# Kernel optimization log

Hardware: AMD Instinct MI355X
Metric: run time of the kernel (lower is better)

The kernel has to match this reference:

```python
import jax, jax.numpy as jnp
import numpy as np

B, C, F, T = 4, 64, 256, 256
CH = C // 2  # self.n_ch inside the module
EPS = 1e-5


def _cbp(x, W, b, g, be, m, v, a):
    # 1x1 conv == channel matmul, then BatchNorm (inference stats) + PReLU (scalar slope)
    y = jnp.einsum('oi,bift->boft', W, x) + b[None, :, None, None]
    y = (y - m[None, :, None, None]) * jax.lax.rsqrt(v[None, :, None, None] + EPS)
    y = y * g[None, :, None, None] + be[None, :, None, None]
    return jnp.where(y > 0, y, a * y)


def setup_inputs() -> dict:
    key = jax.random.key(0)
    ks = jax.random.split(key, 16)

    def conv_params(i, cin, cout, pre):
        W = jax.random.normal(ks[i], (cout, cin), dtype=jnp.float32) * 0.05
        return {
            pre + '_W': W,
            pre + '_b': jnp.zeros((cout,), jnp.float32),
            pre + '_g': jnp.ones((cout,), jnp.float32),
            pre + '_be': jnp.zeros((cout,), jnp.float32),
            pre + '_m': jax.random.normal(ks[i + 1], (cout,), dtype=jnp.float32) * 0.1,
            pre + '_v': jax.random.uniform(ks[i + 2], (cout,), dtype=jnp.float32) + 0.5,
            pre + '_a': jnp.float32(0.25),
        }

    d = {
        'inp': jax.random.normal(ks[12], (B, C, F, T), dtype=jnp.float32),
        'x': jax.random.normal(ks[13], (B, C, F, T), dtype=jnp.float32),
    }
    d.update(conv_params(0, C, 2 * CH, 'fqk'))
    d.update(conv_params(3, C, CH, 'fv'))
    d.update(conv_params(6, C, 2 * CH, 'tqk'))
    d.update(conv_params(9, CH, C, 'proj'))
    return d


def reference(inp, x,
              fqk_W, fqk_b, fqk_g, fqk_be, fqk_m, fqk_v, fqk_a,
              fv_W, fv_b, fv_g, fv_be, fv_m, fv_v, fv_a,
              tqk_W, tqk_b, tqk_g, tqk_be, tqk_m, tqk_v, tqk_a,
              proj_W, proj_b, proj_g, proj_be, proj_m, proj_v, proj_a):
    scale = 1.0 / jnp.sqrt(jnp.float32(CH))

    # frequency attention
    f_qk = _cbp(inp, fqk_W, fqk_b, fqk_g, fqk_be, fqk_m, fqk_v, fqk_a)  # B,2CH,F,T
    vf = _cbp(x, fv_W, fv_b, fv_g, fv_be, fv_m, fv_v, fv_a)             # B,CH,F,T
    r = f_qk.reshape(f_qk.shape[0], CH, 2, F, T)  # 'b (c k) f t -> b c k f t'
    qf, kf = r[:, :, 0], r[:, :, 1]
    f_score = jnp.einsum('bcft,bcyt->btfy', qf, kf) * scale
    f_score = jax.nn.softmax(f_score, axis=-1)
    fout = jnp.einsum('btfy,bcyt->bcft', f_score, vf)

    # time attention (causal mask)
    t_qk = _cbp(inp, tqk_W, tqk_b, tqk_g, tqk_be, tqk_m, tqk_v, tqk_a)
    r = t_qk.reshape(t_qk.shape[0], CH, 2, F, T)
    qt, kt = r[:, :, 0], r[:, :, 1]
    t_score = jnp.einsum('bcft,bcfy->bfty', qt, kt) * scale
    mask = jnp.triu(jnp.ones((T, T), dtype=bool), k=1)  # j - i + 1 with i == j
    neg = -jnp.finfo(t_score.dtype).max
    t_score = jnp.where(mask, neg, t_score)
    t_score = jax.nn.softmax(t_score, axis=-1)
    tout = jnp.einsum('bfty,bcfy->bcft', t_score, fout)

    out = _cbp(tout, proj_W, proj_b, proj_g, proj_be, proj_m, proj_v, proj_a)
    return out + x
```

## Files before the change

kernel.cpp:

```cpp
#include <hip/hip_runtime.h>
#include <hip/hip_bf16.h>

typedef __hip_bfloat16 bf16;
typedef __attribute__((ext_vector_type(8))) short bf16x8;
typedef __attribute__((ext_vector_type(4))) float f32x4;
typedef __attribute__((ext_vector_type(16))) float f32x16;
typedef __attribute__((ext_vector_type(8))) unsigned short u16x8;
typedef __attribute__((ext_vector_type(4))) unsigned int u32x4;
typedef __attribute__((ext_vector_type(2))) unsigned int u32x2;

struct ConvP {
  const float* W; const float* bi; const float* g; const float* be;
  const float* m; const float* v; const float* a;
};

#define QS (0.17677669529663687f * 1.4426950408889634f)

__device__ __forceinline__ unsigned short f2bf(float f) {
  __hip_bfloat16 h = __float2bfloat16(f);
  return __builtin_bit_cast(unsigned short, h);
}
__device__ __forceinline__ float bf2f(unsigned short u) {
  return __uint_as_float(((unsigned)u) << 16);
}
__device__ __forceinline__ float fast_exp2(float x) {
#if __has_builtin(__builtin_amdgcn_exp2f)
  return __builtin_amdgcn_exp2f(x);
#else
  return exp2f(x);
#endif
}

__global__ __launch_bounds__(256, 2) void conv_qkv(
    const float* __restrict__ inp, const float* __restrict__ x,
    ConvP fqk, ConvP fv, ConvP tqk,
    bf16* __restrict__ Qf, bf16* __restrict__ Kf, bf16* __restrict__ Vf,
    bf16* __restrict__ Qt, bf16* __restrict__ Kt)
{
  __shared__ __attribute__((aligned(16))) unsigned short Xb[64 * 260];
  __shared__ __attribute__((aligned(16))) unsigned short S0[256 * 40];
  __shared__ __attribute__((aligned(16))) unsigned short S1[256 * 40];
  __shared__ __attribute__((aligned(8)))  float2 Pc[160];

  const int tid = threadIdx.x;
  const int b = blockIdx.x >> 8;
  const int f = blockIdx.x & 255;
  const size_t gbase = (size_t)b * 64 * 65536 + f * 256;
  const size_t tbase = (size_t)(b * 256 + f) * 8192;

  const int lane = tid & 63;
  const int wid = tid >> 6;
  const int m16 = lane & 15;
  const int quad = lane >> 4;

  if (tid < 160) {
    const ConvP& P = (tid < 64) ? fqk : (tid < 128) ? tqk : fv;
    const int o = (tid < 64) ? tid : (tid < 128) ? tid - 64 : tid - 128;
    float A = P.g[o] * rsqrtf(P.v[o] + 1e-5f);
    float B2 = (P.bi[o] - P.m[o]) * A + P.be[o];
    if (tid < 128 && ((o & 1) == 0)) { A *= QS; B2 *= QS; }
    Pc[tid] = make_float2(A, B2);
  }

  auto load_X = [&](const float* __restrict__ src) {
    #pragma unroll
    for (int r = 0; r < 16; ++r) {
      const int idx = r * 256 + tid;
      const int c = idx >> 6;
      const int t0 = (idx & 63) * 4;
      const float4 v = *(const float4*)(src + gbase + (size_t)c * 65536 + t0);
      unsigned lo = (unsigned)f2bf(v.x) | (((unsigned)f2bf(v.y)) << 16);
      unsigned hi = (unsigned)f2bf(v.z) | (((unsigned)f2bf(v.w)) << 16);
      u32x2 pk = {lo, hi};
      *(u32x2*)&Xb[c * 260 + t0] = pk;
    }
  };

  auto load_A = [&](const float* __restrict__ W, int rowbase, int ks) {
    const float* p = W + (rowbase + m16) * 64 + ks * 32 + quad * 8;
    const float4 lo = *(const float4*)p;
    const float4 hi = *(const float4*)(p + 4);
    bf16x8 r;
    r[0] = (short)f2bf(lo.x); r[1] = (short)f2bf(lo.y);
    r[2] = (short)f2bf(lo.z); r[3] = (short)f2bf(lo.w);
    r[4] = (short)f2bf(hi.x); r[5] = (short)f2bf(hi.y);
    r[6] = (short)f2bf(hi.z); r[7] = (short)f2bf(hi.w);
    return r;
  };

  auto load_B = [&](int tt, int ks) {
    const int t = tt * 16 + m16;
    const int i0 = ks * 32 + quad * 8;
    bf16x8 r;
    #pragma unroll
    for (int j = 0; j < 8; ++j) r[j] = (short)Xb[(i0 + j) * 260 + t];
    return r;
  };

  auto emit = [&](const unsigned short* S, bf16* __restrict__ dst) {
    #pragma unroll
    for (int r = 0; r < 4; ++r) {
      const int chunk = r * 256 + tid;
      const int t = chunk >> 2, part = chunk & 3;
      u32x4 v = *(const u32x4*)&S[t * 40 + part * 8];
      *(u32x4*)(dst + tbase + (size_t)chunk * 8) = v;
    }
  };

  auto leaky = [](float y, float alpha) { return y > 0.f ? y : alpha * y; };

  auto qk_pass = [&](const ConvP& P, int pcb, const bf16x8 (&Bf)[4][2]) {
    bf16x8 A[4][2];
    #pragma unroll
    for (int ot = 0; ot < 4; ++ot)
      #pragma unroll
      for (int ks = 0; ks < 2; ++ks) A[ot][ks] = load_A(P.W, ot * 16, ks);
    float pA[4][4], pB[4][4];
    #pragma unroll
    for (int ot = 0; ot < 4; ++ot)
      #pragma unroll
      for (int r = 0; r < 4; ++r) {
        const float2 pp = Pc[pcb + ot * 16 + quad * 4 + r];
        pA[ot][r] = pp.x; pB[ot][r] = pp.y;
      }
    const float alpha = P.a[0];
    #pragma unroll
    for (int i = 0; i < 4; ++i) {
      const int t = (wid * 4 + i) * 16 + m16;
      #pragma unroll
      for (int ot = 0; ot < 4; ++ot) {
        f32x4 acc = {0.f, 0.f, 0.f, 0.f};
        acc = __builtin_amdgcn_mfma_f32_16x16x32_bf16(A[ot][0], Bf[i][0], acc, 0, 0, 0);
        acc = __builtin_amdgcn_mfma_f32_16x16x32_bf16(A[ot][1], Bf[i][1], acc, 0, 0, 0);
        float y[4];
        #pragma unroll
        for (int r = 0; r < 4; ++r)
          y[r] = leaky(acc[r] * pA[ot][r] + pB[ot][r], alpha);
        const int ch0 = ot * 8 + quad * 2;
        *(unsigned*)&S0[t * 40 + ch0] = (unsigned)f2bf(y[0]) | (((unsigned)f2bf(y[2])) << 16);
        *(unsigned*)&S1[t * 40 + ch0] = (unsigned)f2bf(y[1]) | (((unsigned)f2bf(y[3])) << 16);
      }
    }
  };

  load_X(inp);
  __syncthreads();

  bf16x8 Bf[4][2];
  #pragma unroll
  for (int i = 0; i < 4; ++i)
    #pragma unroll
    for (int ks = 0; ks < 2; ++ks) Bf[i][ks] = load_B(wid * 4 + i, ks);

  qk_pass(fqk, 0, Bf);
  __syncthreads();
  emit(S0, Qf); emit(S1, Kf);
  __syncthreads();
  qk_pass(tqk, 64, Bf);
  __syncthreads();
  emit(S0, Qt); emit(S1, Kt);
  __syncthreads();
  load_X(x);
  __syncthreads();

  {
    bf16x8 A[2][2], Bv[4][2];
    #pragma unroll
    for (int i = 0; i < 4; ++i)
      #pragma unroll
      for (int ks = 0; ks < 2; ++ks) Bv[i][ks] = load_B(wid * 4 + i, ks);
    #pragma unroll
    for (int ot = 0; ot < 2; ++ot)
      #pragma unroll
      for (int ks = 0; ks < 2; ++ks) A[ot][ks] = load_A(fv.W, ot * 16, ks);
    float pA[2][4], pB[2][4];
    #pragma unroll
    for (int ot = 0; ot < 2; ++ot)
      #pragma unroll
      for (int r = 0; r < 4; ++r) {
        const float2 pp = Pc[128 + ot * 16 + quad * 4 + r];
        pA[ot][r] = pp.x; pB[ot][r] = pp.y;
      }
    const float alpha = fv.a[0];
    #pragma unroll
    for (int i = 0; i < 4; ++i) {
      const int t = (wid * 4 + i) * 16 + m16;
      #pragma unroll
      for (int ot = 0; ot < 2; ++ot) {
        f32x4 acc = {0.f, 0.f, 0.f, 0.f};
        acc = __builtin_amdgcn_mfma_f32_16x16x32_bf16(A[ot][0], Bv[i][0], acc, 0, 0, 0);
        acc = __builtin_amdgcn_mfma_f32_16x16x32_bf16(A[ot][1], Bv[i][1], acc, 0, 0, 0);
        float y[4];
        #pragma unroll
        for (int r = 0; r < 4; ++r)
          y[r] = leaky(acc[r] * pA[ot][r] + pB[ot][r], alpha);
        const int ch = ot * 16 + quad * 4;
        *(unsigned*)&S0[t * 40 + ch]     = (unsigned)f2bf(y[0]) | (((unsigned)f2bf(y[1])) << 16);
        *(unsigned*)&S0[t * 40 + ch + 2] = (unsigned)f2bf(y[2]) | (((unsigned)f2bf(y[3])) << 16);
      }
    }
  }
  __syncthreads();
  emit(S0, Vf);
}

template<bool CAUSAL>
__global__ __launch_bounds__(256, 2) void attn_k(
    const bf16* __restrict__ Qg, const bf16* __restrict__ Kg,
    const bf16* __restrict__ Vg, bf16* __restrict__ Og)
{
  __shared__ __attribute__((aligned(16))) unsigned short Kl[256 * 40];
  __shared__ __attribute__((aligned(16))) unsigned short Vt[32 * 264];
  __shared__ __attribute__((aligned(16))) unsigned short Plds[4][16 * 264];
  __shared__ __attribute__((aligned(16))) unsigned short Wsc[4][16 * 40];

  const int inst = blockIdx.x;
  const int b = inst >> 8;
  const int s = inst & 255;
  constexpr int RS = CAUSAL ? 32 : 8192;
  const int qbase = CAUSAL ? inst * 8192 : (b * 2097152 + s * 32);

  const int tid = threadIdx.x;
  #pragma unroll
  for (int k2 = 0; k2 < 4; ++k2) {
    const int chunk = k2 * 256 + tid;
    const int row = chunk >> 2, part = chunk & 3;
    u32x4 val = *(const u32x4*)(Kg + qbase + row * RS + part * 8);
    *(u32x4*)&Kl[row * 40 + part * 8] = val;
  }
  if (tid < 128) {
    const unsigned short* v0 = (const unsigned short*)(Vg + qbase) + (2 * tid) * RS;
    const unsigned short* v1 = v0 + RS;
    u16x8 a[4], c[4];
    #pragma unroll
    for (int q = 0; q < 4; ++q) {
      a[q] = *(const u16x8*)(v0 + 8 * q);
      c[q] = *(const u16x8*)(v1 + 8 * q);
    }
    unsigned int* vt32 = (unsigned int*)Vt;
    #pragma unroll
    for (int cc = 0; cc < 32; ++cc) {
      unsigned lo = a[cc >> 3][cc & 7];
      unsigned hi = c[cc >> 3][cc & 7];
      vt32[(cc * 264 + 2 * tid) >> 1] = lo | (hi << 16);
    }
  }
  __syncthreads();

  const int lane = tid & 63;
  const int wid = tid >> 6;
  const int m16 = lane & 15;
  const int quad = lane >> 4;

  unsigned short* P  = &Plds[wid][0];
  unsigned short* Ws = &Wsc[wid][0];
  const int r4 = lane >> 2, p4 = lane & 3;

  bf16x8 kfr[16];
  #pragma unroll
  for (int ct = 0; ct < 16; ++ct)
    kfr[ct] = *(const bf16x8*)&Kl[(ct * 16 + m16) * 40 + quad * 8];

  #pragma unroll 1
  for (int it = 0; it < 4; ++it) {
    const int rt = wid + 4 * it;
    {
      u32x4 qv = *(const u32x4*)(Qg + qbase + (rt * 16 + r4) * RS + p4 * 8);
      *(u32x4*)&Ws[r4 * 40 + p4 * 8] = qv;
    }
    const bf16x8 qf = *(const bf16x8*)&Ws[m16 * 40 + quad * 8];
    const int nct = CAUSAL ? (rt + 1) : 16;

    f32x4 acc[16];
    #pragma unroll
    for (int ct = 0; ct < 16; ++ct) {
      if (ct < nct) {
        f32x4 z = {0.f, 0.f, 0.f, 0.f};
        acc[ct] = __builtin_amdgcn_mfma_f32_16x16x32_bf16(qf, kfr[ct], z, 0, 0, 0);
      }
    }
    float mx[4] = {-3e38f, -3e38f, -3e38f, -3e38f};
    #pragma unroll
    for (int ct = 0; ct < 16; ++ct) if (ct < nct) {
      #pragma unroll
      for (int r = 0; r < 4; ++r) {
        float v = acc[ct][r];
        if (CAUSAL && (ct == nct - 1) && (m16 > quad * 4 + r)) v = -3e38f;
        acc[ct][r] = v;
        mx[r] = fmaxf(mx[r], v);
      }
    }
    #pragma unroll
    for (int r = 0; r < 4; ++r) {
      float m = mx[r];
      #pragma unroll
      for (int d = 1; d < 16; d <<= 1) m = fmaxf(m, __shfl_xor(m, d, 16));
      mx[r] = m;
    }
    float sum[4] = {0.f, 0.f, 0.f, 0.f};
    #pragma unroll
    for (int ct = 0; ct < 16; ++ct) if (ct < nct) {
      #pragma unroll
      for (int r = 0; r < 4; ++r) {
        float p = fast_exp2(acc[ct][r] - mx[r]);
        acc[ct][r] = p;
        sum[r] += p;
      }
    }
    float inv[4];
    #pragma unroll
    for (int r = 0; r < 4; ++r) {
      float ssum = sum[r];
      #pragma unroll
      for (int d = 1; d < 16; d <<= 1) ssum += __shfl_xor(ssum, d, 16);
      inv[r] = 1.0f / ssum;
    }
    #pragma unroll
    for (int ct = 0; ct < 16; ++ct) if (ct < nct) {
      #pragma unroll
      for (int r = 0; r < 4; ++r)
        P[(quad * 4 + r) * 264 + ct * 16 + m16] = f2bf(acc[ct][r]);
    }
    int ksteps = CAUSAL ? ((rt >> 1) + 1) : 8;
    if (CAUSAL && ((rt & 1) == 0)) {
      #pragma unroll
      for (int u = 0; u < 4; ++u) {
        const int e = lane + 64 * u;
        P[(e >> 4) * 264 + (rt + 1) * 16 + (e & 15)] = 0;
      }
    }
    f32x4 o0 = {0.f, 0.f, 0.f, 0.f}, o1 = {0.f, 0.f, 0.f, 0.f};
    #pragma unroll
    for (int ks = 0; ks < 8; ++ks) {
      if (ks < ksteps) {
        const bf16x8 pf  = *(const bf16x8*)&P[m16 * 264 + ks * 32 + quad * 8];
        const bf16x8 vf0 = *(const bf16x8*)&Vt[m16 * 264 + ks * 32 + quad * 8];
        const bf16x8 vf1 = *(const bf16x8*)&Vt[(16 + m16) * 264 + ks * 32 + quad * 8];
        o0 = __builtin_amdgcn_mfma_f32_16x16x32_bf16(pf, vf0, o0, 0, 0, 0);
        o1 = __builtin_amdgcn_mfma_f32_16x16x32_bf16(pf, vf1, o1, 0, 0, 0);
      }
    }
    #pragma unroll
    for (int r = 0; r < 4; ++r) {
      Ws[(quad * 4 + r) * 40 + m16]      = f2bf(o0[r] * inv[r]);
      Ws[(quad * 4 + r) * 40 + 16 + m16] = f2bf(o1[r] * inv[r]);
    }
    {
      u32x4 ov = *(const u32x4*)&Ws[r4 * 40 + p4 * 8];
      *(u32x4*)(Og + qbase + (rt * 16 + r4) * RS + p4 * 8) = ov;
    }
  }
}

__global__ __launch_bounds__(256) void proj_k(
    const bf16* __restrict__ tout, const float* __restrict__ x,
    ConvP pj, float* __restrict__ out)
{
  __shared__ float2 Pc[64];
  const int tid = threadIdx.x;
  const int b = blockIdx.x >> 8;
  const int f = blockIdx.x & 255;
  if (tid < 64) {
    const float A = pj.g[tid] * rsqrtf(pj.v[tid] + 1e-5f);
    const float B2 = (pj.bi[tid] - pj.m[tid]) * A + pj.be[tid];
    Pc[tid] = make_float2(A, B2);
  }
  const int lane = tid & 63;
  const int wid = tid >> 6;
  const int n32 = lane & 31;
  const int h = lane >> 5;

  bf16x8 Afr[2][2];
  #pragma unroll
  for (int ot = 0; ot < 2; ++ot)
    #pragma unroll
    for (int ks = 0; ks < 2; ++ks) {
      const float* p = pj.W + (ot * 32 + n32) * 32 + ks * 16 + h * 8;
      const float4 lo = *(const float4*)p;
      const float4 hi = *(const float4*)(p + 4);
      bf16x8 r;
      r[0] = (short)f2bf(lo.x); r[1] = (short)f2bf(lo.y);
      r[2] = (short)f2bf(lo.z); r[3] = (short)f2bf(lo.w);
      r[4] = (short)f2bf(hi.x); r[5] = (short)f2bf(hi.y);
      r[6] = (short)f2bf(hi.z); r[7] = (short)f2bf(hi.w);
      Afr[ot][ks] = r;
    }
  __syncthreads();

  const float alpha = pj.a[0];
  const size_t gbase = (size_t)b * 64 * 65536 + f * 256;
  const size_t tbase = (size_t)(b * 256 + f) * 8192;

  #pragma unroll
  for (int tt = 0; tt < 2; ++tt) {
    const int t = wid * 64 + tt * 32 + n32;
    const bf16x8 B0 = *(const bf16x8*)(tout + tbase + (size_t)t * 32 + 0 * 16 + h * 8);
    const bf16x8 B1 = *(const bf16x8*)(tout + tbase + (size_t)t * 32 + 1 * 16 + h * 8);
    #pragma unroll
    for (int ot = 0; ot < 2; ++ot) {
      f32x16 acc = {};
      acc = __builtin_amdgcn_mfma_f32_32x32x16_bf16(Afr[ot][0], B0, acc, 0, 0, 0);
      acc = __builtin_amdgcn_mfma_f32_32x32x16_bf16(Afr[ot][1], B1, acc, 0, 0, 0);
      #pragma unroll
      for (int reg = 0; reg < 16; ++reg) {
        const int o = ot * 32 + (reg & 3) + 8 * (reg >> 2) + 4 * h;
        const float2 pp = Pc[o];
        float y = acc[reg] * pp.x + pp.y;
        y = y > 0.f ? y : alpha * y;
        const size_t off = gbase + (size_t)o * 65536 + t;
        out[off] = y + x[off];
      }
    }
  }
}

extern "C" void kernel_launch(void* const* d_in, const int* in_sizes, int n_in,
                              void* d_out, int out_size, void* d_ws, size_t ws_size,
                              hipStream_t stream) {
  const float* inp = (const float*)d_in[0];
  const float* x   = (const float*)d_in[1];
  auto cp = [&](int i) {
    return ConvP{ (const float*)d_in[i],     (const float*)d_in[i + 1],
                  (const float*)d_in[i + 2], (const float*)d_in[i + 3],
                  (const float*)d_in[i + 4], (const float*)d_in[i + 5],
                  (const float*)d_in[i + 6] };
  };
  ConvP fqk = cp(2), fv = cp(9), tqk = cp(16), pj = cp(23);

  char* ws = (char*)d_ws;
  const size_t SZ = (size_t)4 * 256 * 256 * 32 * 2;
  bf16* Qf = (bf16*)(ws + 0 * SZ);
  bf16* Kf = (bf16*)(ws + 1 * SZ);
  bf16* Vf = (bf16*)(ws + 2 * SZ);
  bf16* Qt = (bf16*)(ws + 3 * SZ);
  bf16* Kt = (bf16*)(ws + 4 * SZ);
  bf16* Ft = (bf16*)(ws + 5 * SZ);
  bf16* To = (bf16*)(ws + 0 * SZ);

  conv_qkv<<<1024, 256, 0, stream>>>(inp, x, fqk, fv, tqk, Qf, Kf, Vf, Qt, Kt);
  attn_k<false><<<1024, 256, 0, stream>>>(Qf, Kf, Vf, Ft);
  attn_k<true><<<1024, 256, 0, stream>>>(Qt, Kt, Ft, To);
  proj_k<<<1024, 256, 0, stream>>>(To, x, pj, (float*)d_out);
}
```

Before: 327.8 us.

## Split conv blocks across time halves and keep attention P in registers

The QKV conv kernel now processes half of the time axis per block, doubling the grid. It uses smaller LDS tiles and per-wave staging buffers, so emits need no block-wide barriers, and it raises the occupancy hint. The attention kernel computes transposed scores (K as the A operand), so each lane holds one query row. This allows a cross-lane reduction with only two shuffles, and the probability fragments are redistributed with shuffles instead of round-tripping through LDS. Q is preloaded straight from global memory, K fragments are read from LDS per tile instead of held in registers, and the LDS footprint shrinks, allowing more blocks per CU at the cost of extra shuffle and permute work.

```diff
diff --git a/kernel.cpp b/kernel.cpp
--- a/kernel.cpp
+++ b/kernel.cpp
@@ -20,8 +20,8 @@
   __hip_bfloat16 h = __float2bfloat16(f);
   return __builtin_bit_cast(unsigned short, h);
 }
-__device__ __forceinline__ float bf2f(unsigned short u) {
-  return __uint_as_float(((unsigned)u) << 16);
+__device__ __forceinline__ unsigned pack2(float a, float b) {
+  return (unsigned)f2bf(a) | (((unsigned)f2bf(b)) << 16);
 }
 __device__ __forceinline__ float fast_exp2(float x) {
 #if __has_builtin(__builtin_amdgcn_exp2f)
@@ -31,26 +31,26 @@
 #endif
 }
 
-__global__ __launch_bounds__(256, 2) void conv_qkv(
+__global__ __launch_bounds__(256, 4) void conv_qkv(
     const float* __restrict__ inp, const float* __restrict__ x,
     ConvP fqk, ConvP fv, ConvP tqk,
     bf16* __restrict__ Qf, bf16* __restrict__ Kf, bf16* __restrict__ Vf,
     bf16* __restrict__ Qt, bf16* __restrict__ Kt)
 {
-  __shared__ __attribute__((aligned(16))) unsigned short Xb[64 * 260];
-  __shared__ __attribute__((aligned(16))) unsigned short S0[256 * 40];
-  __shared__ __attribute__((aligned(16))) unsigned short S1[256 * 40];
+  __shared__ __attribute__((aligned(16))) unsigned short Xb[64 * 132];
+  __shared__ __attribute__((aligned(16))) unsigned short Sw[4][2][32 * 40];
   __shared__ __attribute__((aligned(8)))  float2 Pc[160];
 
   const int tid = threadIdx.x;
-  const int b = blockIdx.x >> 8;
-  const int f = blockIdx.x & 255;
-  const size_t gbase = (size_t)b * 64 * 65536 + f * 256;
-  const size_t tbase = (size_t)(b * 256 + f) * 8192;
+  const int b  = blockIdx.x >> 9;
+  const int f  = (blockIdx.x >> 1) & 255;
+  const int th = blockIdx.x & 1;
+  const size_t gsrc = (size_t)b * 64 * 65536 + (size_t)f * 256 + th * 128;
+  const size_t tb   = ((size_t)(b * 256 + f) * 256 + th * 128) * 32;
 
   const int lane = tid & 63;
-  const int wid = tid >> 6;
-  const int m16 = lane & 15;
+  const int wid  = tid >> 6;
+  const int m16  = lane & 15;
   const int quad = lane >> 4;
 
   if (tid < 160) {
@@ -64,15 +64,13 @@
 
   auto load_X = [&](const float* __restrict__ src) {
     #pragma unroll
-    for (int r = 0; r < 16; ++r) {
+    for (int r = 0; r < 8; ++r) {
       const int idx = r * 256 + tid;
-      const int c = idx >> 6;
-      const int t0 = (idx & 63) * 4;
-      const float4 v = *(const float4*)(src + gbase + (size_t)c * 65536 + t0);
-      unsigned lo = (unsigned)f2bf(v.x) | (((unsigned)f2bf(v.y)) << 16);
-      unsigned hi = (unsigned)f2bf(v.z) | (((unsigned)f2bf(v.w)) << 16);
-      u32x2 pk = {lo, hi};
-      *(u32x2*)&Xb[c * 260 + t0] = pk;
+      const int c = idx >> 5;
+      const int tl = (idx & 31) * 4;
+      const float4 v = *(const float4*)(src + gsrc + (size_t)c * 65536 + tl);
+      u32x2 pk = {pack2(v.x, v.y), pack2(v.z, v.w)};
+      *(u32x2*)&Xb[c * 132 + tl] = pk;
     }
   };
 
@@ -88,45 +86,51 @@
     return r;
   };
 
-  auto load_B = [&](int tt, int ks) {
-    const int t = tt * 16 + m16;
+  auto load_B = [&](int i, int ks) {
+    const int t = (2 * wid + i) * 16 + m16;
     const int i0 = ks * 32 + quad * 8;
     bf16x8 r;
     #pragma unroll
-    for (int j = 0; j < 8; ++j) r[j] = (short)Xb[(i0 + j) * 260 + t];
+    for (int j = 0; j < 8; ++j) r[j] = (short)Xb[(i0 + j) * 132 + t];
     return r;
   };
 
-  auto emit = [&](const unsigned short* S, bf16* __restrict__ dst) {
-    #pragma unroll
-    for (int r = 0; r < 4; ++r) {
-      const int chunk = r * 256 + tid;
-      const int t = chunk >> 2, part = chunk & 3;
-      u32x4 v = *(const u32x4*)&S[t * 40 + part * 8];
-      *(u32x4*)(dst + tbase + (size_t)chunk * 8) = v;
+  auto emitw = [&](const unsigned short* S, bf16* __restrict__ dst) {
+    #pragma unroll
+    for (int k = 0; k < 2; ++k) {
+      const int chunk = k * 64 + lane;
+      const int tloc = chunk >> 2, part = chunk & 3;
+      u32x4 v = *(const u32x4*)&S[tloc * 40 + part * 8];
+      *(u32x4*)(dst + tb + (size_t)wid * 1024 + (size_t)chunk * 8) = v;
     }
   };
 
   auto leaky = [](float y, float alpha) { return y > 0.f ? y : alpha * y; };
 
-  auto qk_pass = [&](const ConvP& P, int pcb, const bf16x8 (&Bf)[4][2]) {
+  load_X(inp);
+  __syncthreads();
+
+  bf16x8 Bf[2][2];
+  #pragma unroll
+  for (int i = 0; i < 2; ++i)
+    #pragma unroll
+    for (int ks = 0; ks < 2; ++ks) Bf[i][ks] = load_B(i, ks);
+
+  #pragma unroll 1
+  for (int which = 0; which < 2; ++which) {
+    const ConvP& P = which ? tqk : fqk;
+    const int pcb = which ? 64 : 0;
     bf16x8 A[4][2];
     #pragma unroll
     for (int ot = 0; ot < 4; ++ot)
       #pragma unroll
       for (int ks = 0; ks < 2; ++ks) A[ot][ks] = load_A(P.W, ot * 16, ks);
-    float pA[4][4], pB[4][4];
-    #pragma unroll
-    for (int ot = 0; ot < 4; ++ot)
-      #pragma unroll
-      for (int r = 0; r < 4; ++r) {
-        const float2 pp = Pc[pcb + ot * 16 + quad * 4 + r];
-        pA[ot][r] = pp.x; pB[ot][r] = pp.y;
-      }
     const float alpha = P.a[0];
-    #pragma unroll
-    for (int i = 0; i < 4; ++i) {
-      const int t = (wid * 4 + i) * 16 + m16;
+    unsigned short* SwQ = &Sw[wid][0][0];
+    unsigned short* SwK = &Sw[wid][1][0];
+    #pragma unroll
+    for (int i = 0; i < 2; ++i) {
+      const int tloc = i * 16 + m16;
       #pragma unroll
       for (int ot = 0; ot < 4; ++ot) {
         f32x4 acc = {0.f, 0.f, 0.f, 0.f};
@@ -134,57 +138,39 @@
         acc = __builtin_amdgcn_mfma_f32_16x16x32_bf16(A[ot][1], Bf[i][1], acc, 0, 0, 0);
         float y[4];
         #pragma unroll
-        for (int r = 0; r < 4; ++r)
-          y[r] = leaky(acc[r] * pA[ot][r] + pB[ot][r], alpha);
+        for (int r = 0; r < 4; ++r) {
+          const float2 pp = Pc[pcb + ot * 16 + quad * 4 + r];
+          y[r] = leaky(acc[r] * pp.x + pp.y, alpha);
+        }
         const int ch0 = ot * 8 + quad * 2;
-        *(unsigned*)&S0[t * 40 + ch0] = (unsigned)f2bf(y[0]) | (((unsigned)f2bf(y[2])) << 16);
-        *(unsigned*)&S1[t * 40 + ch0] = (unsigned)f2bf(y[1]) | (((unsigned)f2bf(y[3])) << 16);
-      }
-    }
-  };
-
-  load_X(inp);
-  __syncthreads();
-
-  bf16x8 Bf[4][2];
-  #pragma unroll
-  for (int i = 0; i < 4; ++i)
-    #pragma unroll
-    for (int ks = 0; ks < 2; ++ks) Bf[i][ks] = load_B(wid * 4 + i, ks);
-
-  qk_pass(fqk, 0, Bf);
-  __syncthreads();
-  emit(S0, Qf); emit(S1, Kf);
-  __syncthreads();
-  qk_pass(tqk, 64, Bf);
-  __syncthreads();
-  emit(S0, Qt); emit(S1, Kt);
+        *(unsigned*)&SwQ[tloc * 40 + ch0] = pack2(y[0], y[2]);
+        *(unsigned*)&SwK[tloc * 40 + ch0] = pack2(y[1], y[3]);
+      }
+    }
+    emitw(SwQ, which ? Qt : Qf);
+    emitw(SwK, which ? Kt : Kf);
+  }
+
   __syncthreads();
   load_X(x);
   __syncthreads();
 
   {
-    bf16x8 A[2][2], Bv[4][2];
-    #pragma unroll
-    for (int i = 0; i < 4; ++i)
-      #pragma unroll
-      for (int ks = 0; ks < 2; ++ks) Bv[i][ks] = load_B(wid * 4 + i, ks);
+    bf16x8 Bv[2][2];
+    #pragma unroll
+    for (int i = 0; i < 2; ++i)
+      #pragma unroll
+      for (int ks = 0; ks < 2; ++ks) Bv[i][ks] = load_B(i, ks);
+    bf16x8 A[2][2];
     #pragma unroll
     for (int ot = 0; ot < 2; ++ot)
       #pragma unroll
       for (int ks = 0; ks < 2; ++ks) A[ot][ks] = load_A(fv.W, ot * 16, ks);
-    float pA[2][4], pB[2][4];
-    #pragma unroll
-    for (int ot = 0; ot < 2; ++ot)
-      #pragma unroll
-      for (int r = 0; r < 4; ++r) {
-        const float2 pp = Pc[128 + ot * 16 + quad * 4 + r];
-        pA[ot][r] = pp.x; pB[ot][r] = pp.y;
-      }
     const float alpha = fv.a[0];
-    #pragma unroll
-    for (int i = 0; i < 4; ++i) {
-      const int t = (wid * 4 + i) * 16 + m16;
+    unsigned short* SwV = &Sw[wid][0][0];
+    #pragma unroll
+    for (int i = 0; i < 2; ++i) {
+      const int tloc = i * 16 + m16;
       #pragma unroll
       for (int ot = 0; ot < 2; ++ot) {
         f32x4 acc = {0.f, 0.f, 0.f, 0.f};
@@ -192,27 +178,26 @@
         acc = __builtin_amdgcn_mfma_f32_16x16x32_bf16(A[ot][1], Bv[i][1], acc, 0, 0, 0);
         float y[4];
         #pragma unroll
-        for (int r = 0; r < 4; ++r)
-          y[r] = leaky(acc[r] * pA[ot][r] + pB[ot][r], alpha);
+        for (int r = 0; r < 4; ++r) {
+          const float2 pp = Pc[128 + ot * 16 + quad * 4 + r];
+          y[r] = leaky(acc[r] * pp.x + pp.y, alpha);
+        }
         const int ch = ot * 16 + quad * 4;
-        *(unsigned*)&S0[t * 40 + ch]     = (unsigned)f2bf(y[0]) | (((unsigned)f2bf(y[1])) << 16);
-        *(unsigned*)&S0[t * 40 + ch + 2] = (unsigned)f2bf(y[2]) | (((unsigned)f2bf(y[3])) << 16);
-      }
-    }
-  }
-  __syncthreads();
-  emit(S0, Vf);
+        *(unsigned*)&SwV[tloc * 40 + ch]     = pack2(y[0], y[1]);
+        *(unsigned*)&SwV[tloc * 40 + ch + 2] = pack2(y[2], y[3]);
+      }
+    }
+    emitw(SwV, Vf);
+  }
 }
 
 template<bool CAUSAL>
-__global__ __launch_bounds__(256, 2) void attn_k(
+__global__ __launch_bounds__(256, 3) void attn_k(
     const bf16* __restrict__ Qg, const bf16* __restrict__ Kg,
     const bf16* __restrict__ Vg, bf16* __restrict__ Og)
 {
   __shared__ __attribute__((aligned(16))) unsigned short Kl[256 * 40];
   __shared__ __attribute__((aligned(16))) unsigned short Vt[32 * 264];
-  __shared__ __attribute__((aligned(16))) unsigned short Plds[4][16 * 264];
-  __shared__ __attribute__((aligned(16))) unsigned short Wsc[4][16 * 40];
 
   const int inst = blockIdx.x;
   const int b = inst >> 8;
@@ -221,6 +206,20 @@
   const int qbase = CAUSAL ? inst * 8192 : (b * 2097152 + s * 32);
 
   const int tid = threadIdx.x;
+  const int lane = tid & 63;
+  const int wid = tid >> 6;
+  const int m16 = lane & 15;
+  const int quad = lane >> 4;
+  const int qh = quad >> 1;
+  const int ql = quad & 1;
+
+  bf16x8 qfr[4];
+  #pragma unroll
+  for (int it = 0; it < 4; ++it) {
+    const int rt = wid + 4 * it;
+    qfr[it] = *(const bf16x8*)(Qg + qbase + (rt * 16 + m16) * RS + quad * 8);
+  }
+
   #pragma unroll
   for (int k2 = 0; k2 < 4; ++k2) {
     const int chunk = k2 * 256 + tid;
@@ -242,113 +241,91 @@
     for (int cc = 0; cc < 32; ++cc) {
       unsigned lo = a[cc >> 3][cc & 7];
       unsigned hi = c[cc >> 3][cc & 7];
-      vt32[(cc * 264 + 2 * tid) >> 1] = lo | (hi << 16);
+      vt32[cc * 132 + tid] = lo | (hi << 16);
     }
   }
   __syncthreads();
-
-  const int lane = tid & 63;
-  const int wid = tid >> 6;
-  const int m16 = lane & 15;
-  const int quad = lane >> 4;
-
-  unsigned short* P  = &Plds[wid][0];
-  unsigned short* Ws = &Wsc[wid][0];
-  const int r4 = lane >> 2, p4 = lane & 3;
-
-  bf16x8 kfr[16];
-  #pragma unroll
-  for (int ct = 0; ct < 16; ++ct)
-    kfr[ct] = *(const bf16x8*)&Kl[(ct * 16 + m16) * 40 + quad * 8];
 
   #pragma unroll 1
   for (int it = 0; it < 4; ++it) {
     const int rt = wid + 4 * it;
-    {
-      u32x4 qv = *(const u32x4*)(Qg + qbase + (rt * 16 + r4) * RS + p4 * 8);
-      *(u32x4*)&Ws[r4 * 40 + p4 * 8] = qv;
-    }
-    const bf16x8 qf = *(const bf16x8*)&Ws[m16 * 40 + quad * 8];
+    const bf16x8 qf = qfr[it];
     const int nct = CAUSAL ? (rt + 1) : 16;
 
     f32x4 acc[16];
     #pragma unroll
     for (int ct = 0; ct < 16; ++ct) {
       if (ct < nct) {
+        const bf16x8 kf = *(const bf16x8*)&Kl[(ct * 16 + m16) * 40 + quad * 8];
         f32x4 z = {0.f, 0.f, 0.f, 0.f};
-        acc[ct] = __builtin_amdgcn_mfma_f32_16x16x32_bf16(qf, kfr[ct], z, 0, 0, 0);
-      }
-    }
-    float mx[4] = {-3e38f, -3e38f, -3e38f, -3e38f};
+        acc[ct] = __builtin_amdgcn_mfma_f32_16x16x32_bf16(kf, qf, z, 0, 0, 0);
+      }
+    }
+    float mx = -3e38f;
     #pragma unroll
     for (int ct = 0; ct < 16; ++ct) if (ct < nct) {
       #pragma unroll
       for (int r = 0; r < 4; ++r) {
         float v = acc[ct][r];
-        if (CAUSAL && (ct == nct - 1) && (m16 > quad * 4 + r)) v = -3e38f;
+        if (CAUSAL && (ct == rt) && (quad * 4 + r > m16)) v = -1e30f;
         acc[ct][r] = v;
-        mx[r] = fmaxf(mx[r], v);
-      }
-    }
-    #pragma unroll
-    for (int r = 0; r < 4; ++r) {
-      float m = mx[r];
-      #pragma unroll
-      for (int d = 1; d < 16; d <<= 1) m = fmaxf(m, __shfl_xor(m, d, 16));
-      mx[r] = m;
-    }
-    float sum[4] = {0.f, 0.f, 0.f, 0.f};
+        mx = fmaxf(mx, v);
+      }
+    }
+    mx = fmaxf(mx, __shfl_xor(mx, 16));
+    mx = fmaxf(mx, __shfl_xor(mx, 32));
+
+    float sum = 0.f;
+    uint2 pk[16];
     #pragma unroll
     for (int ct = 0; ct < 16; ++ct) if (ct < nct) {
-      #pragma unroll
-      for (int r = 0; r < 4; ++r) {
-        float p = fast_exp2(acc[ct][r] - mx[r]);
-        acc[ct][r] = p;
-        sum[r] += p;
-      }
-    }
-    float inv[4];
-    #pragma unroll
-    for (int r = 0; r < 4; ++r) {
-      float ssum = sum[r];
-      #pragma unroll
-      for (int d = 1; d < 16; d <<= 1) ssum += __shfl_xor(ssum, d, 16);
-      inv[r] = 1.0f / ssum;
-    }
-    #pragma unroll
-    for (int ct = 0; ct < 16; ++ct) if (ct < nct) {
-      #pragma unroll
-      for (int r = 0; r < 4; ++r)
-        P[(quad * 4 + r) * 264 + ct * 16 + m16] = f2bf(acc[ct][r]);
-    }
-    int ksteps = CAUSAL ? ((rt >> 1) + 1) : 8;
-    if (CAUSAL && ((rt & 1) == 0)) {
-      #pragma unroll
-      for (int u = 0; u < 4; ++u) {
-        const int e = lane + 64 * u;
-        P[(e >> 4) * 264 + (rt + 1) * 16 + (e & 15)] = 0;
-      }
-    }
+      float p0 = fast_exp2(acc[ct][0] - mx);
+      float p1 = fast_exp2(acc[ct][1] - mx);
+      float p2 = fast_exp2(acc[ct][2] - mx);
+      float p3 = fast_exp2(acc[ct][3] - mx);
+      sum += (p0 + p1) + (p2 + p3);
+      pk[ct].x = pack2(p0, p1);
+      pk[ct].y = pack2(p2, p3);
+    }
+    if (CAUSAL && ((rt & 1) == 0)) { pk[rt + 1].x = 0u; pk[rt + 1].y = 0u; }
+    sum += __shfl_xor(sum, 16);
+    sum += __shfl_xor(sum, 32);
+    const float inv = 1.0f / sum;
+
     f32x4 o0 = {0.f, 0.f, 0.f, 0.f}, o1 = {0.f, 0.f, 0.f, 0.f};
+    const int ksteps = CAUSAL ? ((rt >> 1) + 1) : 8;
+    const int srcA = m16 + 16 * (2 * ql + qh);
+    const int srcB = m16 + 16 * (2 * ql + (qh ^ 1));
     #pragma unroll
     for (int ks = 0; ks < 8; ++ks) {
       if (ks < ksteps) {
-        const bf16x8 pf  = *(const bf16x8*)&P[m16 * 264 + ks * 32 + quad * 8];
-        const bf16x8 vf0 = *(const bf16x8*)&Vt[m16 * 264 + ks * 32 + quad * 8];
-        const bf16x8 vf1 = *(const bf16x8*)&Vt[(16 + m16) * 264 + ks * 32 + quad * 8];
-        o0 = __builtin_amdgcn_mfma_f32_16x16x32_bf16(pf, vf0, o0, 0, 0, 0);
-        o1 = __builtin_amdgcn_mfma_f32_16x16x32_bf16(pf, vf1, o1, 0, 0, 0);
-      }
-    }
-    #pragma unroll
-    for (int r = 0; r < 4; ++r) {
-      Ws[(quad * 4 + r) * 40 + m16]      = f2bf(o0[r] * inv[r]);
-      Ws[(quad * 4 + r) * 40 + 16 + m16] = f2bf(o1[r] * inv[r]);
-    }
-    {
-      u32x4 ov = *(const u32x4*)&Ws[r4 * 40 + p4 * 8];
-      *(u32x4*)(Og + qbase + (rt * 16 + r4) * RS + p4 * 8) = ov;
-    }
+        const uint2 cA = pk[2 * ks + ql];
+        const uint2 cB = pk[2 * ks + (ql ^ 1)];
+        u32x4 pf;
+        pf[0] = (unsigned)__shfl((int)cA.x, srcA);
+        pf[1] = (unsigned)__shfl((int)cA.y, srcA);
+        pf[2] = (unsigned)__shfl((int)cB.x, srcB);
+        pf[3] = (unsigned)__shfl((int)cB.y, srcB);
+        const bf16x8 pfrag = __builtin_bit_cast(bf16x8, pf);
+        #pragma unroll
+        for (int c = 0; c < 2; ++c) {
+          u32x4 vv = *(const u32x4*)&Vt[(c * 16 + m16) * 264 + ks * 32 + qh * 16 + ql * 8];
+          u32x4 vs;
+          vs[0] = qh ? vv[2] : vv[0];
+          vs[1] = qh ? vv[3] : vv[1];
+          vs[2] = qh ? vv[0] : vv[2];
+          vs[3] = qh ? vv[1] : vv[3];
+          const bf16x8 vfrag = __builtin_bit_cast(bf16x8, vs);
+          if (c == 0) o0 = __builtin_amdgcn_mfma_f32_16x16x32_bf16(vfrag, pfrag, o0, 0, 0, 0);
+          else        o1 = __builtin_amdgcn_mfma_f32_16x16x32_bf16(vfrag, pfrag, o1, 0, 0, 0);
+        }
+      }
+    }
+    const size_t obase = qbase + (size_t)(rt * 16 + m16) * RS;
+    u32x2 s0 = {pack2(o0[0] * inv, o0[1] * inv), pack2(o0[2] * inv, o0[3] * inv)};
+    u32x2 s1 = {pack2(o1[0] * inv, o1[1] * inv), pack2(o1[2] * inv, o1[3] * inv)};
+    *(u32x2*)(Og + obase + quad * 4)      = s0;
+    *(u32x2*)(Og + obase + 16 + quad * 4) = s1;
   }
 }
 
@@ -437,7 +414,7 @@
   bf16* Ft = (bf16*)(ws + 5 * SZ);
   bf16* To = (bf16*)(ws + 0 * SZ);
 
-  conv_qkv<<<1024, 256, 0, stream>>>(inp, x, fqk, fv, tqk, Qf, Kf, Vf, Qt, Kt);
+  conv_qkv<<<2048, 256, 0, stream>>>(inp, x, fqk, fv, tqk, Qf, Kf, Vf, Qt, Kt);
   attn_k<false><<<1024, 256, 0, stream>>>(Qf, Kf, Vf, Ft);
   attn_k<true><<<1024, 256, 0, stream>>>(Qt, Kt, Ft, To);
   proj_k<<<1024, 256, 0, stream>>>(To, x, pj, (float*)d_out);
```

Result: slower. 466.3 us (+42.3%).
